# Optimization experiments

Hardware: AMD Instinct MI355X
Metric: run time of the kernel (lower is better)

Reference implementation:

```python
import jax, jax.numpy as jnp
import numpy as np

TOP_K = 2


def setup_inputs() -> dict:
    key = jax.random.key(0)
    k0, k1, k2, k3, k4 = jax.random.split(key, 5)
    B, S, H, I, E = 4, 2048, 1024, 2816, 8
    s_h = 1.0 / np.sqrt(H)
    s_i = 1.0 / np.sqrt(I)
    return {
        "x": jax.random.normal(k0, (B, S, H), jnp.float32),
        # nn.Linear weights are stored as [out_features, in_features]
        "w_router": jax.random.normal(k1, (E, H), jnp.float32) * s_h,   # gate: H -> E
        "w_gate": jax.random.normal(k2, (E, I, H), jnp.float32) * s_h,  # per-expert gate_proj
        "w_up": jax.random.normal(k3, (E, I, H), jnp.float32) * s_h,    # per-expert up_proj
        "w_down": jax.random.normal(k4, (E, H, I), jnp.float32) * s_i,  # per-expert down_proj
    }


def reference(x, w_router, w_gate, w_up, w_down):
    B, S, H = x.shape
    E = w_router.shape[0]
    xf = x.reshape(-1, H)                      # [T, H], T = B*S

    # --- Router: softmax over experts, top-k, renormalize weights ---
    logits = jnp.einsum("th,eh->te", xf, w_router)        # [T, E]
    probs = jax.nn.softmax(logits, axis=-1)
    topw, topi = jax.lax.top_k(probs, TOP_K)              # [T, k]
    topw = topw / jnp.sum(topw, axis=-1, keepdims=True)

    # Per-token combine weight for each expert: sum_k w[t,k] * 1[idx[t,k]==e]
    onehot = (topi[..., None] == jnp.arange(E)).astype(x.dtype)  # [T, k, E]
    combine = jnp.einsum("tk,tke->te", topw, onehot)             # [T, E]

    # --- Experts: SwiGLU MLP per expert on all tokens, masked combine ---
    # (masked-dense in the original == gather-compute mathematically,
    # since silu(0)*0 = 0 and the projections have no bias)
    gate = jax.nn.silu(jnp.einsum("th,eih->eti", xf, w_gate))    # [E, T, I]
    up = jnp.einsum("th,eih->eti", xf, w_up)                     # [E, T, I]
    down = jnp.einsum("eti,ehi->eth", gate * up, w_down)         # [E, T, H]

    out = jnp.einsum("eth,te->th", down, combine)                # [T, H]
    return out.reshape(B, S, H)
```

## Files before the change

kernel.cpp:

```cpp
#include <hip/hip_runtime.h>

#define TT 8192
#define HD 1024
#define ID 2816
#define NE 8
#define NID2 (2*ID)

typedef __attribute__((ext_vector_type(8))) short short8;
typedef __attribute__((ext_vector_type(4))) float f32x4;

#define WS_TOP2I 0
#define WS_TOP2W 65536
#define WS_CNT   131072
#define WS_OFF   131136
#define WS_CUR   131200
#define WS_TMAP  131328
#define WS_SLOTW 196864
#define WS_T2S   262400
#define WS_XB    1048576ULL
#define WS_WGU   (WS_XB  + 16777216ULL)
#define WS_WDB   (WS_WGU + 92274688ULL)
#define WS_ACT   (WS_WDB + 46137344ULL)

__device__ __forceinline__ unsigned int pack_bf2(float lo, float hi) {
  unsigned int ul = __builtin_bit_cast(unsigned int, lo) + 0x8000u;
  unsigned int uh = __builtin_bit_cast(unsigned int, hi) + 0x8000u;
  return (uh & 0xffff0000u) | (ul >> 16);
}

__device__ __forceinline__ unsigned short f2bf(float f) {
  unsigned int u = __builtin_bit_cast(unsigned int, f);
  return (unsigned short)((u + 0x8000u) >> 16);
}

__device__ __forceinline__ void gload16(const void* g, void* l) {
  __builtin_amdgcn_global_load_lds(
      (const __attribute__((address_space(1))) unsigned int*)g,
      (__attribute__((address_space(3))) unsigned int*)l, 16, 0, 0);
}

__global__ __launch_bounds__(256) void router_kernel(
    const float* __restrict__ x, const float* __restrict__ wr,
    int* __restrict__ top2i, float* __restrict__ top2w,
    unsigned short* __restrict__ xb)
{
  int tid  = threadIdx.x;
  int lane = tid & 63;
  int t    = blockIdx.x * 4 + (tid >> 6);

  const float4* xp = (const float4*)(x + (size_t)t * HD + lane * 16);
  float4 xv[4];
  #pragma unroll
  for (int j = 0; j < 4; ++j) xv[j] = xp[j];

  uint4 v0, v1;
  v0.x = pack_bf2(xv[0].x, xv[0].y); v0.y = pack_bf2(xv[0].z, xv[0].w);
  v0.z = pack_bf2(xv[1].x, xv[1].y); v0.w = pack_bf2(xv[1].z, xv[1].w);
  v1.x = pack_bf2(xv[2].x, xv[2].y); v1.y = pack_bf2(xv[2].z, xv[2].w);
  v1.z = pack_bf2(xv[3].x, xv[3].y); v1.w = pack_bf2(xv[3].z, xv[3].w);
  uint4* xrow = (uint4*)(xb + (size_t)t * HD + lane * 16);
  xrow[0] = v0; xrow[1] = v1;

  float acc[NE];
  #pragma unroll
  for (int e = 0; e < NE; ++e) {
    const float4* wp = (const float4*)(wr + (size_t)e * HD + lane * 16);
    float s = 0.f;
    #pragma unroll
    for (int j = 0; j < 4; ++j) {
      float4 w = wp[j];
      s += xv[j].x * w.x + xv[j].y * w.y + xv[j].z * w.z + xv[j].w * w.w;
    }
    acc[e] = s;
  }
  #pragma unroll
  for (int d = 1; d < 64; d <<= 1) {
    #pragma unroll
    for (int e = 0; e < NE; ++e) acc[e] += __shfl_xor(acc[e], d, 64);
  }
  int   i0 = 0; float m0 = acc[0];
  #pragma unroll
  for (int e = 1; e < NE; ++e) if (acc[e] > m0) { m0 = acc[e]; i0 = e; }
  int   i1 = -1; float m1 = -3.4e38f;
  #pragma unroll
  for (int e = 0; e < NE; ++e) if (e != i0 && acc[e] > m1) { m1 = acc[e]; i1 = e; }

  float e1 = __expf(m1 - m0);
  float w0 = 1.f / (1.f + e1);
  float w1 = e1 * w0;

  if (lane == 0) {
    top2i[2 * t] = i0;  top2i[2 * t + 1] = i1;
    top2w[2 * t] = w0;  top2w[2 * t + 1] = w1;
  }
}

__global__ __launch_bounds__(256) void count_scan_kernel(
    const int* __restrict__ top2i,
    int* __restrict__ counts, int* __restrict__ offsets, int* __restrict__ cursors)
{
  __shared__ int s_cnt[NE];
  int tid = threadIdx.x;
  if (tid < NE) s_cnt[tid] = 0;
  __syncthreads();

  int c0=0,c1=0,c2=0,c3=0,c4=0,c5=0,c6=0,c7=0;
  for (int t = tid; t < TT; t += 256) {
    int e0 = top2i[2 * t], e1 = top2i[2 * t + 1];
    c0 += __popcll(__ballot(e0 == 0)) + __popcll(__ballot(e1 == 0));
    c1 += __popcll(__ballot(e0 == 1)) + __popcll(__ballot(e1 == 1));
    c2 += __popcll(__ballot(e0 == 2)) + __popcll(__ballot(e1 == 2));
    c3 += __popcll(__ballot(e0 == 3)) + __popcll(__ballot(e1 == 3));
    c4 += __popcll(__ballot(e0 == 4)) + __popcll(__ballot(e1 == 4));
    c5 += __popcll(__ballot(e0 == 5)) + __popcll(__ballot(e1 == 5));
    c6 += __popcll(__ballot(e0 == 6)) + __popcll(__ballot(e1 == 6));
    c7 += __popcll(__ballot(e0 == 7)) + __popcll(__ballot(e1 == 7));
  }
  if ((tid & 63) == 0) {
    atomicAdd(&s_cnt[0], c0); atomicAdd(&s_cnt[1], c1);
    atomicAdd(&s_cnt[2], c2); atomicAdd(&s_cnt[3], c3);
    atomicAdd(&s_cnt[4], c4); atomicAdd(&s_cnt[5], c5);
    atomicAdd(&s_cnt[6], c6); atomicAdd(&s_cnt[7], c7);
  }
  __syncthreads();
  if (tid == 0) {
    int run = 0;
    #pragma unroll
    for (int e = 0; e < NE; ++e) {
      counts[e] = s_cnt[e]; offsets[e] = run; cursors[e] = run; run += s_cnt[e];
    }
    offsets[NE] = run;
  }
}

__global__ __launch_bounds__(256) void place_kernel(
    const int* __restrict__ top2i, const float* __restrict__ top2w,
    int* __restrict__ cursors,
    int* __restrict__ token_map, float* __restrict__ slot_w, int* __restrict__ tok2slot)
{
  int tid  = threadIdx.x;
  int lane = tid & 63;
  int t    = blockIdx.x * 256 + tid;

  #pragma unroll
  for (int k = 0; k < 2; ++k) {
    int   e = top2i[2 * t + k];
    float w = top2w[2 * t + k];
    #pragma unroll
    for (int ee = 0; ee < NE; ++ee) {
      unsigned long long m = __ballot(e == ee);
      if (e == ee) {
        int leader = __ffsll((long long)m) - 1;
        int pre    = __popcll(m & ((1ull << lane) - 1ull));
        int base   = 0;
        if (lane == leader) base = atomicAdd(&cursors[ee], (int)__popcll(m));
        base = __shfl(base, leader, 64);
        token_map[base + pre] = t;
        slot_w[base + pre]    = w;
        tok2slot[2 * t + k]   = base + pre;
      }
    }
  }
}

__global__ __launch_bounds__(256) void cvt_wgu_kernel(
    const float* __restrict__ wg, const float* __restrict__ wu,
    unsigned short* __restrict__ wgu)
{
  int e   = blockIdx.y;
  int idx = blockIdx.x * 256 + threadIdx.x;
  int col8 = idx & 127;
  int rr   = idx >> 7;
  int blk  = rr >> 8;
  int win  = rr & 255;
  const float* srow = (win < 128)
      ? wg + ((size_t)e * ID + blk * 128 + win) * HD
      : wu + ((size_t)e * ID + blk * 128 + (win - 128)) * HD;
  const float4* p = (const float4*)(srow + col8 * 8);
  float4 a = p[0], b = p[1];
  uint4 v;
  v.x = pack_bf2(a.x, a.y); v.y = pack_bf2(a.z, a.w);
  v.z = pack_bf2(b.x, b.y); v.w = pack_bf2(b.z, b.w);
  *(uint4*)(wgu + ((size_t)e * NID2 + rr) * HD + col8 * 8) = v;
}

__global__ __launch_bounds__(256) void cvt_bf16_kernel(
    const float* __restrict__ in, unsigned short* __restrict__ out, int n8)
{
  int i = blockIdx.x * 256 + threadIdx.x;
  if (i >= n8) return;
  const float4* p = (const float4*)(in + (size_t)i * 8);
  float4 a = p[0], b = p[1];
  uint4 v;
  v.x = pack_bf2(a.x, a.y); v.y = pack_bf2(a.z, a.w);
  v.z = pack_bf2(b.x, b.y); v.w = pack_bf2(b.z, b.w);
  ((uint4*)out)[i] = v;
}


#define STAGE8(t) { \
    size_t k1 = (size_t)((t) * 64); \
    char* db = ldsc + (((t) & 1) ? 65536u : 0u) + (unsigned)tid * 16; \
    gload16(aS[0] + k1, db);           gload16(aS[1] + k1, db + 8192); \
    gload16(aS[2] + k1, db + 16384);   gload16(aS[3] + k1, db + 24576); \
    gload16(bS[0] + k1, db + 32768);   gload16(bS[1] + k1, db + 40960); \
    gload16(bS[2] + k1, db + 49152);   gload16(bS[3] + k1, db + 57344); }

#define KTILE_BODY(t, NKT) { \
    if ((t) + 1 < (NKT)) STAGE8((t) + 1); \
    const char* sa = ldsc + (((t) & 1) ? 65536u : 0u); \
    const char* sb = sa + 32768; \
    _Pragma("unroll") for (int kk = 0; kk < 2; ++kk) { \
      int kb = kk * 64 + kq; \
      short8 bfr[4], af[8]; \
      _Pragma("unroll") for (int n = 0; n < 4; ++n) \
        bfr[n] = *(const short8*)(sb + (wc * 64 + n * 16 + arow) * 128 + (kb ^ rxor)); \
      _Pragma("unroll") for (int m = 0; m < 8; ++m) \
        af[m] = *(const short8*)(sa + (wr * 128 + m * 16 + arow) * 128 + (kb ^ rxor)); \
      __builtin_amdgcn_s_setprio(1); \
      _Pragma("unroll") for (int m = 0; m < 8; ++m) \
        _Pragma("unroll") for (int n = 0; n < 4; ++n) \
          acc[m][n] = __builtin_amdgcn_mfma_f32_16x16x32_bf16(af[m], bfr[n], acc[m][n], 0, 0, 0); \
      __builtin_amdgcn_s_setprio(0); \
    } \
    asm volatile("s_waitcnt vmcnt(0)" ::: "memory"); \
    __builtin_amdgcn_s_barrier(); }

#define XCD_DECODE(NX, NY) \
  int nwg  = (NX) * (NY) * NE; \
  int flat = blockIdx.x + (NX) * (blockIdx.y + (NY) * blockIdx.z); \
  int qq   = nwg >> 3; \
  int wg   = (flat & 7) * qq + (flat >> 3); \
  int bx   = wg % (NX); \
  int rem  = wg / (NX); \
  int y    = rem % (NY); \
  int e    = rem / (NY);

__global__ __launch_bounds__(512, 2) void gemm1_fast(
    const unsigned short* __restrict__ xb, const unsigned short* __restrict__ wgu,
    const int* __restrict__ counts, const int* __restrict__ offsets,
    const int* __restrict__ token_map, unsigned short* __restrict__ act)
{
  extern __shared__ char smem[];
  char* ldsc = smem;

  XCD_DECODE(16, 22)
  int cnt = counts[e];
  int off = offsets[e];

  int tid  = threadIdx.x;
  int lane = tid & 63;
  int w    = tid >> 6;
  int wr   = w >> 2;
  int wc   = w & 3;

  int srow0 = tid >> 3;
  int colE  = (((tid & 7) ^ ((tid >> 3) & 7)) << 3);
  int rxor  = (lane & 7) << 4;
  int arow  = lane & 15;
  int kq    = (lane >> 4) << 4;
  int prow  = (lane >> 4) << 2;

  for (int t0 = bx * 256; t0 < cnt; t0 += 4096) {
    const unsigned short* aS[4];
    const unsigned short* bS[4];
    #pragma unroll
    for (int j = 0; j < 4; ++j) {
      int row  = srow0 + 64 * j;
      int tr   = t0 + row;
      int slot = off + (tr < cnt ? tr : cnt - 1);
      aS[j] = xb  + (size_t)token_map[slot] * HD + colE;
      bS[j] = wgu + ((size_t)e * NID2 + (size_t)y * 256 + row) * HD + colE;
    }

    f32x4 zf = {0.f, 0.f, 0.f, 0.f};
    f32x4 acc[8][4];
    #pragma unroll
    for (int m = 0; m < 8; ++m)
      #pragma unroll
      for (int n = 0; n < 4; ++n) acc[m][n] = zf;

    STAGE8(0);
    asm volatile("s_waitcnt vmcnt(0)" ::: "memory");
    __builtin_amdgcn_s_barrier();
    for (int t = 0; t < HD / 64; ++t) KTILE_BODY(t, HD / 64);

    __syncthreads();
    float* xch = (float*)smem;
    if (wc >= 2) {
      float* base = xch + (size_t)((wr * 2 + (wc - 2)) * 8192);
      #pragma unroll
      for (int m = 0; m < 8; ++m)
        #pragma unroll
        for (int n = 0; n < 4; ++n)
          #pragma unroll
          for (int r = 0; r < 4; ++r)
            base[(m * 16 + prow + r) * 64 + n * 16 + arow] = acc[m][n][r];
    }
    __syncthreads();
    if (wc < 2) {
      const float* base = xch + (size_t)((wr * 2 + wc) * 8192);
      int i0 = y * 128 + wc * 64;
      #pragma unroll
      for (int m = 0; m < 8; ++m) {
        #pragma unroll
        for (int r = 0; r < 4; ++r) {
          int row = wr * 128 + m * 16 + prow + r;
          int tr2 = t0 + row;
          if (tr2 >= cnt) continue;
          size_t ob = (size_t)(off + tr2) * ID + i0 + arow;
          #pragma unroll
          for (int n = 0; n < 4; ++n) {
            float g = acc[m][n][r];
            float u = base[(m * 16 + prow + r) * 64 + n * 16 + arow];
            float h = g * u / (1.f + __expf(-g));
            act[ob + n * 16] = f2bf(h);
          }
        }
      }
    }
    __syncthreads();
  }
}

__global__ __launch_bounds__(512, 2) void gemm2_fast(
    const unsigned short* __restrict__ act, const unsigned short* __restrict__ wdb,
    const int* __restrict__ counts, const int* __restrict__ offsets,
    float* __restrict__ down)
{
  extern __shared__ char smem[];
  char* ldsc = smem;

  XCD_DECODE(16, 4)
  int cnt = counts[e];
  int off = offsets[e];

  int tid  = threadIdx.x;
  int lane = tid & 63;
  int w    = tid >> 6;
  int wr   = w >> 2;
  int wc   = w & 3;

  int srow0 = tid >> 3;
  int colE  = (((tid & 7) ^ ((tid >> 3) & 7)) << 3);
  int rxor  = (lane & 7) << 4;
  int arow  = lane & 15;
  int kq    = (lane >> 4) << 4;
  int prow  = (lane >> 4) << 2;

  for (int t0 = bx * 256; t0 < cnt; t0 += 4096) {
    const unsigned short* aS[4];
    const unsigned short* bS[4];
    #pragma unroll
    for (int j = 0; j < 4; ++j) {
      int row  = srow0 + 64 * j;
      int tr   = t0 + row;
      int slot = off + (tr < cnt ? tr : cnt - 1);
      aS[j] = act + (size_t)slot * ID + colE;
      bS[j] = wdb + ((size_t)e * HD + (size_t)y * 256 + row) * ID + colE;
    }

    f32x4 zf = {0.f, 0.f, 0.f, 0.f};
    f32x4 acc[8][4];
    #pragma unroll
    for (int m = 0; m < 8; ++m)
      #pragma unroll
      for (int n = 0; n < 4; ++n) acc[m][n] = zf;

    STAGE8(0);
    asm volatile("s_waitcnt vmcnt(0)" ::: "memory");
    __builtin_amdgcn_s_barrier();
    for (int t = 0; t < ID / 64; ++t) KTILE_BODY(t, ID / 64);

    #pragma unroll
    for (int m = 0; m < 8; ++m) {
      #pragma unroll
      for (int r = 0; r < 4; ++r) {
        int row = wr * 128 + m * 16 + prow + r;
        int tr2 = t0 + row;
        if (tr2 >= cnt) continue;
        float* ob = down + (size_t)(off + tr2) * HD + (size_t)y * 256 + wc * 64 + arow;
        #pragma unroll
        for (int n = 0; n < 4; ++n)
          ob[n * 16] = acc[m][n][r];
      }
    }
  }
}

__global__ __launch_bounds__(256) void combine_kernel(
    const float* __restrict__ down, const float* __restrict__ slot_w,
    const int* __restrict__ tok2slot, float* __restrict__ out)
{
  int t   = blockIdx.x;
  int tid = threadIdx.x;
  int s0  = tok2slot[2 * t], s1 = tok2slot[2 * t + 1];
  float w0 = slot_w[s0], w1 = slot_w[s1];
  const float4* d0 = (const float4*)(down + (size_t)s0 * HD) + tid;
  const float4* d1 = (const float4*)(down + (size_t)s1 * HD) + tid;
  float4 a = *d0, b = *d1;
  float4 o;
  o.x = w0 * a.x + w1 * b.x;  o.y = w0 * a.y + w1 * b.y;
  o.z = w0 * a.z + w1 * b.z;  o.w = w0 * a.w + w1 * b.w;
  ((float4*)(out + (size_t)t * HD))[tid] = o;
}

extern "C" void kernel_launch(void* const* d_in, const int* in_sizes, int n_in,
                              void* d_out, int out_size, void* d_ws, size_t ws_size,
                              hipStream_t stream) {
  const float* x        = (const float*)d_in[0];
  const float* w_router = (const float*)d_in[1];
  const float* w_gate   = (const float*)d_in[2];
  const float* w_up     = (const float*)d_in[3];
  const float* w_down   = (const float*)d_in[4];

  char* ws = (char*)d_ws;
  int*   top2i    = (int*)(ws + WS_TOP2I);
  float* top2w    = (float*)(ws + WS_TOP2W);
  int*   counts   = (int*)(ws + WS_CNT);
  int*   offsets  = (int*)(ws + WS_OFF);
  int*   cursors  = (int*)(ws + WS_CUR);
  int*   tmap     = (int*)(ws + WS_TMAP);
  float* slotw    = (float*)(ws + WS_SLOTW);
  int*   tok2slot = (int*)(ws + WS_T2S);
  unsigned short* xb  = (unsigned short*)(ws + WS_XB);
  unsigned short* wgu = (unsigned short*)(ws + WS_WGU);
  unsigned short* wdb = (unsigned short*)(ws + WS_WDB);
  unsigned short* act = (unsigned short*)(ws + WS_ACT);
  float*          down = (float*)(ws + WS_WGU);

  hipFuncSetAttribute((const void*)gemm1_fast,
                      hipFuncAttributeMaxDynamicSharedMemorySize, 131072);
  hipFuncSetAttribute((const void*)gemm2_fast,
                      hipFuncAttributeMaxDynamicSharedMemorySize, 131072);

  router_kernel<<<TT / 4, 256, 0, stream>>>(x, w_router, top2i, top2w, xb);
  count_scan_kernel<<<1, 256, 0, stream>>>(top2i, counts, offsets, cursors);
  place_kernel<<<TT / 256, 256, 0, stream>>>(top2i, top2w, cursors, tmap, slotw, tok2slot);
  cvt_wgu_kernel<<<dim3(2816, NE), 256, 0, stream>>>(w_gate, w_up, wgu);
  cvt_bf16_kernel<<<11264, 256, 0, stream>>>(w_down, wdb, NE * HD * ID / 8);

  gemm1_fast<<<dim3(16, 22, NE), 512, 131072, stream>>>(xb, wgu, counts, offsets, tmap, act);
  gemm2_fast<<<dim3(16, 4, NE), 512, 131072, stream>>>(act, wdb, counts, offsets, down);
  combine_kernel<<<TT, 256, 0, stream>>>(down, slotw, tok2slot, (float*)d_out);
}
```

Measured before the change: 583.4 us.

## Interleave next-tile global loads across four MFMA phases and halve grid x-dimension

The K-tile loop is restructured so that prefetch of the next tile is split into four two-load groups, each issued between MFMA quarter-blocks. Partial vmcnt waits let compute start on B rows 0-1 before all loads land, replacing the full drain at the end of every tile. The grid's token dimension is also halved from 16 to 8 blocks per expert, so each block loops over more token tiles with stride 2048, and gemm2 gets a trailing syncthreads between iterations. The aim is to hide global-to-LDS latency behind MFMA work and cut per-tile barrier stalls, at the cost of fewer resident blocks and more iterations per block.

```diff
diff --git a/kernel.cpp b/kernel.cpp
--- a/kernel.cpp
+++ b/kernel.cpp
@@ -198,33 +198,56 @@
 }
 
 
-#define STAGE8(t) { \
-    size_t k1 = (size_t)((t) * 64); \
-    char* db = ldsc + (((t) & 1) ? 65536u : 0u) + (unsigned)tid * 16; \
-    gload16(aS[0] + k1, db);           gload16(aS[1] + k1, db + 8192); \
-    gload16(aS[2] + k1, db + 16384);   gload16(aS[3] + k1, db + 24576); \
-    gload16(bS[0] + k1, db + 32768);   gload16(bS[1] + k1, db + 40960); \
-    gload16(bS[2] + k1, db + 49152);   gload16(bS[3] + k1, db + 57344); }
-
-#define KTILE_BODY(t, NKT) { \
-    if ((t) + 1 < (NKT)) STAGE8((t) + 1); \
+#define ISSUE2(t1, j0, j1, SRC, DOFF) { \
+    size_t k1 = (size_t)((t1) * 64); \
+    char* db = ldsc + (((t1) & 1) ? 65536u : 0u) + (unsigned)tid * 16 + (DOFF); \
+    gload16(SRC[j0] + k1, db + (j0) * 8192); \
+    gload16(SRC[j1] + k1, db + (j1) * 8192); }
+
+#define ISSUE_B01(t1) ISSUE2(t1, 0, 1, bS, 32768u)
+#define ISSUE_B23(t1) ISSUE2(t1, 2, 3, bS, 32768u)
+#define ISSUE_A02(t1) ISSUE2(t1, 0, 2, aS, 0u)
+#define ISSUE_A13(t1) ISSUE2(t1, 1, 3, aS, 0u)
+
+#define MFMA16(MBASE) \
+    __builtin_amdgcn_s_setprio(1); \
+    _Pragma("unroll") for (int m = 0; m < 4; ++m) \
+      _Pragma("unroll") for (int n = 0; n < 4; ++n) \
+        acc[(MBASE) + m][n] = __builtin_amdgcn_mfma_f32_16x16x32_bf16(af[m], bfr[n], acc[(MBASE) + m][n], 0, 0, 0); \
+    __builtin_amdgcn_s_setprio(0);
+
+#define KTILE(t, ISSUE, N1STR) { \
     const char* sa = ldsc + (((t) & 1) ? 65536u : 0u); \
     const char* sb = sa + 32768; \
-    _Pragma("unroll") for (int kk = 0; kk < 2; ++kk) { \
-      int kb = kk * 64 + kq; \
-      short8 bfr[4], af[8]; \
-      _Pragma("unroll") for (int n = 0; n < 4; ++n) \
-        bfr[n] = *(const short8*)(sb + (wc * 64 + n * 16 + arow) * 128 + (kb ^ rxor)); \
-      _Pragma("unroll") for (int m = 0; m < 8; ++m) \
-        af[m] = *(const short8*)(sa + (wr * 128 + m * 16 + arow) * 128 + (kb ^ rxor)); \
-      __builtin_amdgcn_s_setprio(1); \
-      _Pragma("unroll") for (int m = 0; m < 8; ++m) \
-        _Pragma("unroll") for (int n = 0; n < 4; ++n) \
-          acc[m][n] = __builtin_amdgcn_mfma_f32_16x16x32_bf16(af[m], bfr[n], acc[m][n], 0, 0, 0); \
-      __builtin_amdgcn_s_setprio(0); \
-    } \
-    asm volatile("s_waitcnt vmcnt(0)" ::: "memory"); \
-    __builtin_amdgcn_s_barrier(); }
+    short8 bfr[4], af[4]; \
+     \
+    asm volatile("s_waitcnt vmcnt(2)" ::: "memory"); \
+    __builtin_amdgcn_s_barrier(); \
+    if (ISSUE) ISSUE_B01((t) + 1); \
+    _Pragma("unroll") for (int n = 0; n < 4; ++n) \
+      bfr[n] = *(const short8*)(sb + (wc * 64 + n * 16 + arow) * 128 + (kq ^ rxor)); \
+    _Pragma("unroll") for (int m = 0; m < 4; ++m) \
+      af[m] = *(const short8*)(sa + (wr * 128 + m * 16 + arow) * 128 + (kq ^ rxor)); \
+    MFMA16(0) \
+     \
+    asm volatile("s_waitcnt vmcnt(" N1STR ")" ::: "memory"); \
+    __builtin_amdgcn_s_barrier(); \
+    if (ISSUE) ISSUE_B23((t) + 1); \
+    _Pragma("unroll") for (int m = 0; m < 4; ++m) \
+      af[m] = *(const short8*)(sa + (wr * 128 + 64 + m * 16 + arow) * 128 + (kq ^ rxor)); \
+    MFMA16(4) \
+     \
+    if (ISSUE) ISSUE_A02((t) + 1); \
+    _Pragma("unroll") for (int n = 0; n < 4; ++n) \
+      bfr[n] = *(const short8*)(sb + (wc * 64 + n * 16 + arow) * 128 + ((64 + kq) ^ rxor)); \
+    _Pragma("unroll") for (int m = 0; m < 4; ++m) \
+      af[m] = *(const short8*)(sa + (wr * 128 + m * 16 + arow) * 128 + ((64 + kq) ^ rxor)); \
+    MFMA16(0) \
+     \
+    if (ISSUE) ISSUE_A13((t) + 1); \
+    _Pragma("unroll") for (int m = 0; m < 4; ++m) \
+      af[m] = *(const short8*)(sa + (wr * 128 + 64 + m * 16 + arow) * 128 + ((64 + kq) ^ rxor)); \
+    MFMA16(4) }
 
 #define XCD_DECODE(NX, NY) \
   int nwg  = (NX) * (NY) * NE; \
@@ -244,7 +267,7 @@
   extern __shared__ char smem[];
   char* ldsc = smem;
 
-  XCD_DECODE(16, 22)
+  XCD_DECODE(8, 22)
   int cnt = counts[e];
   int off = offsets[e];
 
@@ -261,7 +284,7 @@
   int kq    = (lane >> 4) << 4;
   int prow  = (lane >> 4) << 2;
 
-  for (int t0 = bx * 256; t0 < cnt; t0 += 4096) {
+  for (int t0 = bx * 256; t0 < cnt; t0 += 2048) {
     const unsigned short* aS[4];
     const unsigned short* bS[4];
     #pragma unroll
@@ -280,10 +303,9 @@
       #pragma unroll
       for (int n = 0; n < 4; ++n) acc[m][n] = zf;
 
-    STAGE8(0);
-    asm volatile("s_waitcnt vmcnt(0)" ::: "memory");
-    __builtin_amdgcn_s_barrier();
-    for (int t = 0; t < HD / 64; ++t) KTILE_BODY(t, HD / 64);
+    ISSUE_B01(0); ISSUE_B23(0); ISSUE_A02(0); ISSUE_A13(0);
+    for (int t = 0; t < HD / 64 - 1; ++t) KTILE(t, true, "2");
+    KTILE(HD / 64 - 1, false, "0");
 
     __syncthreads();
     float* xch = (float*)smem;
@@ -331,7 +353,7 @@
   extern __shared__ char smem[];
   char* ldsc = smem;
 
-  XCD_DECODE(16, 4)
+  XCD_DECODE(8, 4)
   int cnt = counts[e];
   int off = offsets[e];
 
@@ -348,7 +370,7 @@
   int kq    = (lane >> 4) << 4;
   int prow  = (lane >> 4) << 2;
 
-  for (int t0 = bx * 256; t0 < cnt; t0 += 4096) {
+  for (int t0 = bx * 256; t0 < cnt; t0 += 2048) {
     const unsigned short* aS[4];
     const unsigned short* bS[4];
     #pragma unroll
@@ -367,10 +389,9 @@
       #pragma unroll
       for (int n = 0; n < 4; ++n) acc[m][n] = zf;
 
-    STAGE8(0);
-    asm volatile("s_waitcnt vmcnt(0)" ::: "memory");
-    __builtin_amdgcn_s_barrier();
-    for (int t = 0; t < ID / 64; ++t) KTILE_BODY(t, ID / 64);
+    ISSUE_B01(0); ISSUE_B23(0); ISSUE_A02(0); ISSUE_A13(0);
+    for (int t = 0; t < ID / 64 - 1; ++t) KTILE(t, true, "2");
+    KTILE(ID / 64 - 1, false, "0");
 
     #pragma unroll
     for (int m = 0; m < 8; ++m) {
@@ -385,6 +406,7 @@
           ob[n * 16] = acc[m][n][r];
       }
     }
+    __syncthreads();
   }
 }
 
@@ -440,7 +462,7 @@
   cvt_wgu_kernel<<<dim3(2816, NE), 256, 0, stream>>>(w_gate, w_up, wgu);
   cvt_bf16_kernel<<<11264, 256, 0, stream>>>(w_down, wdb, NE * HD * ID / 8);
 
-  gemm1_fast<<<dim3(16, 22, NE), 512, 131072, stream>>>(xb, wgu, counts, offsets, tmap, act);
-  gemm2_fast<<<dim3(16, 4, NE), 512, 131072, stream>>>(act, wdb, counts, offsets, down);
+  gemm1_fast<<<dim3(8, 22, NE), 512, 131072, stream>>>(xb, wgu, counts, offsets, tmap, act);
+  gemm2_fast<<<dim3(8, 4, NE), 512, 131072, stream>>>(act, wdb, counts, offsets, down);
   combine_kernel<<<TT, 256, 0, stream>>>(down, slotw, tok2slot, (float*)d_out);
 }
```

Result: faster. 564.8 us (-3.2%).

## Use four-stage K=32 LDS pipeline and halve GEMM grid width

Applied to the files above, without the earlier changes.

Replaces the double-buffered K=64 staging in both expert GEMMs with a 4-buffer ring of K=32 tiles, three tiles in flight. Partial vmcnt waits replace the full drain each iteration, so global loads overlap MFMA work more deeply. The LDS swizzle is adjusted for 64-byte rows. The grid x-dimension drops from 16 to 8 with a matching token stride, so each workgroup handles more token tiles and fewer CTAs are launched. This risks lower occupancy and imbalance across experts, and a trailing sync is added in gemm2 to keep the buffer reuse across tiles safe.

```diff
diff --git a/kernel.cpp b/kernel.cpp
--- a/kernel.cpp
+++ b/kernel.cpp
@@ -198,33 +198,36 @@
 }
 
 
-#define STAGE8(t) { \
-    size_t k1 = (size_t)((t) * 64); \
-    char* db = ldsc + (((t) & 1) ? 65536u : 0u) + (unsigned)tid * 16; \
-    gload16(aS[0] + k1, db);           gload16(aS[1] + k1, db + 8192); \
-    gload16(aS[2] + k1, db + 16384);   gload16(aS[3] + k1, db + 24576); \
-    gload16(bS[0] + k1, db + 32768);   gload16(bS[1] + k1, db + 40960); \
-    gload16(bS[2] + k1, db + 49152);   gload16(bS[3] + k1, db + 57344); }
-
-#define KTILE_BODY(t, NKT) { \
-    if ((t) + 1 < (NKT)) STAGE8((t) + 1); \
-    const char* sa = ldsc + (((t) & 1) ? 65536u : 0u); \
-    const char* sb = sa + 32768; \
-    _Pragma("unroll") for (int kk = 0; kk < 2; ++kk) { \
-      int kb = kk * 64 + kq; \
-      short8 bfr[4], af[8]; \
+#define VW(N) asm volatile("s_waitcnt vmcnt(" #N ")" ::: "memory")
+#define BAR() __builtin_amdgcn_s_barrier()
+
+#define ISSUE(t) { \
+    size_t k1 = (size_t)((t) * 32); \
+    char* db = ldsc + (((t) & 3) * 32768u) + (unsigned)tid * 16; \
+    gload16(aS[0] + k1, db);            gload16(aS[1] + k1, db + 8192); \
+    gload16(bS[0] + k1, db + 16384);    gload16(bS[1] + k1, db + 24576); }
+
+#define BODY(t) { \
+    const char* sa = ldsc + (((t) & 3) * 32768u); \
+    const char* sb = sa + 16384; \
+    short8 af[8], bfr[4]; \
+    _Pragma("unroll") for (int n = 0; n < 4; ++n) \
+      bfr[n] = *(const short8*)(sb + (wc * 64 + n * 16 + arow) * 64 + kx); \
+    _Pragma("unroll") for (int m = 0; m < 8; ++m) \
+      af[m] = *(const short8*)(sa + (wr * 128 + m * 16 + arow) * 64 + kx); \
+    __builtin_amdgcn_s_setprio(1); \
+    _Pragma("unroll") for (int m = 0; m < 8; ++m) \
       _Pragma("unroll") for (int n = 0; n < 4; ++n) \
-        bfr[n] = *(const short8*)(sb + (wc * 64 + n * 16 + arow) * 128 + (kb ^ rxor)); \
-      _Pragma("unroll") for (int m = 0; m < 8; ++m) \
-        af[m] = *(const short8*)(sa + (wr * 128 + m * 16 + arow) * 128 + (kb ^ rxor)); \
-      __builtin_amdgcn_s_setprio(1); \
-      _Pragma("unroll") for (int m = 0; m < 8; ++m) \
-        _Pragma("unroll") for (int n = 0; n < 4; ++n) \
-          acc[m][n] = __builtin_amdgcn_mfma_f32_16x16x32_bf16(af[m], bfr[n], acc[m][n], 0, 0, 0); \
-      __builtin_amdgcn_s_setprio(0); \
-    } \
-    asm volatile("s_waitcnt vmcnt(0)" ::: "memory"); \
-    __builtin_amdgcn_s_barrier(); }
+        acc[m][n] = __builtin_amdgcn_mfma_f32_16x16x32_bf16(af[m], bfr[n], acc[m][n], 0, 0, 0); \
+    __builtin_amdgcn_s_setprio(0); }
+
+#define KLOOP(NT) { \
+    ISSUE(0); ISSUE(1); ISSUE(2); \
+    int t = 0; \
+    for (; t < (NT) - 3; ++t) { VW(8); BAR(); ISSUE(t + 3); BODY(t); } \
+    VW(8); BAR(); BODY(t); ++t; \
+    VW(4); BAR(); BODY(t); ++t; \
+    VW(0); BAR(); BODY(t); }
 
 #define XCD_DECODE(NX, NY) \
   int nwg  = (NX) * (NY) * NE; \
@@ -244,7 +247,7 @@
   extern __shared__ char smem[];
   char* ldsc = smem;
 
-  XCD_DECODE(16, 22)
+  XCD_DECODE(8, 22)
   int cnt = counts[e];
   int off = offsets[e];
 
@@ -254,19 +257,18 @@
   int wr   = w >> 2;
   int wc   = w & 3;
 
-  int srow0 = tid >> 3;
-  int colE  = (((tid & 7) ^ ((tid >> 3) & 7)) << 3);
-  int rxor  = (lane & 7) << 4;
-  int arow  = lane & 15;
-  int kq    = (lane >> 4) << 4;
-  int prow  = (lane >> 4) << 2;
-
-  for (int t0 = bx * 256; t0 < cnt; t0 += 4096) {
-    const unsigned short* aS[4];
-    const unsigned short* bS[4];
-    #pragma unroll
-    for (int j = 0; j < 4; ++j) {
-      int row  = srow0 + 64 * j;
+  int srow = tid >> 2;
+  int colE = (((tid & 3) ^ ((tid >> 2) & 3)) << 3);
+  int arow = lane & 15;
+  int kx   = (((lane >> 4) ^ (lane & 3)) << 4);
+  int prow = (lane >> 4) << 2;
+
+  for (int t0 = bx * 256; t0 < cnt; t0 += 2048) {
+    const unsigned short* aS[2];
+    const unsigned short* bS[2];
+    #pragma unroll
+    for (int j = 0; j < 2; ++j) {
+      int row  = srow + 128 * j;
       int tr   = t0 + row;
       int slot = off + (tr < cnt ? tr : cnt - 1);
       aS[j] = xb  + (size_t)token_map[slot] * HD + colE;
@@ -280,10 +282,7 @@
       #pragma unroll
       for (int n = 0; n < 4; ++n) acc[m][n] = zf;
 
-    STAGE8(0);
-    asm volatile("s_waitcnt vmcnt(0)" ::: "memory");
-    __builtin_amdgcn_s_barrier();
-    for (int t = 0; t < HD / 64; ++t) KTILE_BODY(t, HD / 64);
+    KLOOP(HD / 32);
 
     __syncthreads();
     float* xch = (float*)smem;
@@ -331,7 +330,7 @@
   extern __shared__ char smem[];
   char* ldsc = smem;
 
-  XCD_DECODE(16, 4)
+  XCD_DECODE(8, 4)
   int cnt = counts[e];
   int off = offsets[e];
 
@@ -341,19 +340,18 @@
   int wr   = w >> 2;
   int wc   = w & 3;
 
-  int srow0 = tid >> 3;
-  int colE  = (((tid & 7) ^ ((tid >> 3) & 7)) << 3);
-  int rxor  = (lane & 7) << 4;
-  int arow  = lane & 15;
-  int kq    = (lane >> 4) << 4;
-  int prow  = (lane >> 4) << 2;
-
-  for (int t0 = bx * 256; t0 < cnt; t0 += 4096) {
-    const unsigned short* aS[4];
-    const unsigned short* bS[4];
-    #pragma unroll
-    for (int j = 0; j < 4; ++j) {
-      int row  = srow0 + 64 * j;
+  int srow = tid >> 2;
+  int colE = (((tid & 3) ^ ((tid >> 2) & 3)) << 3);
+  int arow = lane & 15;
+  int kx   = (((lane >> 4) ^ (lane & 3)) << 4);
+  int prow = (lane >> 4) << 2;
+
+  for (int t0 = bx * 256; t0 < cnt; t0 += 2048) {
+    const unsigned short* aS[2];
+    const unsigned short* bS[2];
+    #pragma unroll
+    for (int j = 0; j < 2; ++j) {
+      int row  = srow + 128 * j;
       int tr   = t0 + row;
       int slot = off + (tr < cnt ? tr : cnt - 1);
       aS[j] = act + (size_t)slot * ID + colE;
@@ -367,10 +365,7 @@
       #pragma unroll
       for (int n = 0; n < 4; ++n) acc[m][n] = zf;
 
-    STAGE8(0);
-    asm volatile("s_waitcnt vmcnt(0)" ::: "memory");
-    __builtin_amdgcn_s_barrier();
-    for (int t = 0; t < ID / 64; ++t) KTILE_BODY(t, ID / 64);
+    KLOOP(ID / 32);
 
     #pragma unroll
     for (int m = 0; m < 8; ++m) {
@@ -385,6 +380,7 @@
           ob[n * 16] = acc[m][n][r];
       }
     }
+    __syncthreads();
   }
 }
 
@@ -440,7 +436,7 @@
   cvt_wgu_kernel<<<dim3(2816, NE), 256, 0, stream>>>(w_gate, w_up, wgu);
   cvt_bf16_kernel<<<11264, 256, 0, stream>>>(w_down, wdb, NE * HD * ID / 8);
 
-  gemm1_fast<<<dim3(16, 22, NE), 512, 131072, stream>>>(xb, wgu, counts, offsets, tmap, act);
-  gemm2_fast<<<dim3(16, 4, NE), 512, 131072, stream>>>(act, wdb, counts, offsets, down);
+  gemm1_fast<<<dim3(8, 22, NE), 512, 131072, stream>>>(xb, wgu, counts, offsets, tmap, act);
+  gemm2_fast<<<dim3(8, 4, NE), 512, 131072, stream>>>(act, wdb, counts, offsets, down);
   combine_kernel<<<TT, 256, 0, stream>>>(down, slotw, tok2slot, (float*)d_out);
 }
```

After: 654.2 us. 1.12x slower.
